# Optimization experiments

Measured on AMD Instinct MI355X. Metric: run time of the kernel, lower is better.

## Reference

```python
import jax, jax.numpy as jnp
import numpy as np

EPS = 1e-08


def _d_hat(d, mask, eps=EPS):
    # d: [B,N,H,W] float, mask: [B,N,H,W] bool
    B, N, H, W = mask.shape
    flat_d = d.reshape(B * N, H * W)
    flat_m = mask.reshape(B * N, H * W)
    cnt = flat_m.sum(axis=1)  # [BN] int
    # masked median: push invalid entries to +inf, sort, pick lower-median index
    sorted_v = jnp.sort(jnp.where(flat_m, flat_d, jnp.inf), axis=1)
    idx = jnp.maximum((cnt - 1) // 2, 0)
    med = jnp.take_along_axis(sorted_v, idx[:, None], axis=1)[:, 0]
    med = jnp.where(cnt > 0, med, jnp.zeros_like(med))  # empty mask -> median 0
    cnt_f = jnp.maximum(cnt, 1).astype(d.dtype)
    # masked MAD scale (mean abs deviation over valid pixels) + eps
    abs_sum = (jnp.abs(flat_d - med[:, None]) * flat_m).sum(axis=1)
    sc = jnp.where(cnt > 0, abs_sum / cnt_f + eps, jnp.full_like(abs_sum, eps))
    d_hat = (flat_d - med[:, None]) / sc[:, None]
    return d_hat.reshape(B, N, H, W)


def _avg_pool(x, k):
    # matches F.avg_pool2d(x, k, stride=k): crop to full windows, mean per kxk block
    B, N, H, W = x.shape
    Hk, Wk = H // k, W // k
    xc = x[..., : Hk * k, : Wk * k].reshape(B, N, Hk, k, Wk, k)
    return xc.mean(axis=(3, 5))


def _grad_loss(pred, target, mask):
    total = jnp.asarray(0.0, pred.dtype)
    mf = mask.astype(pred.dtype)
    for s in range(4):
        if s == 0:
            p, t, m = pred, target, mask
        else:
            k = 2 ** s
            p = _avg_pool(pred, k)
            t = _avg_pool(target, k)
            m = _avg_pool(mf, k) > 0  # .bool() of pooled float mask
        diff = p - t
        gx = jnp.abs(diff[..., :, 1:] - diff[..., :, :-1])
        gy = jnp.abs(diff[..., 1:, :] - diff[..., :-1, :])
        mx = m[..., :, 1:] & m[..., :, :-1]
        my = m[..., 1:, :] & m[..., :-1, :]
        lx = (gx * mx).sum() / jnp.maximum(mx.sum(), 1).astype(pred.dtype)
        ly = (gy * my).sum() / jnp.maximum(my.sum(), 1).astype(pred.dtype)
        total = total + lx + ly
    return total / 4


def setup_inputs() -> dict:
    key = jax.random.key(0)
    k1, k2, k3 = jax.random.split(key, 3)
    B, N, H, W = 4, 16, 518, 518
    pred = jax.random.normal(k1, (B, N, H, W), dtype=jnp.float32)
    y = jax.random.normal(k2, (B, N, H, W), dtype=jnp.float32)
    masks_squeezed = jax.random.bernoulli(k3, 0.9, (B, N, H, W))
    return {"pred": pred, "y": y, "masks_squeezed": masks_squeezed}


def reference(pred, y, masks_squeezed):
    mask = masks_squeezed.astype(bool)
    pred_hat = _d_hat(pred, mask)
    y_hat = _d_hat(y, mask)
    rho = jnp.abs(pred_hat - y_hat) * mask  # rho[~mask] = 0
    valid = jnp.maximum(mask.sum(axis=(2, 3)).astype(pred.dtype), 1.0)
    loss_ssi = (rho.sum(axis=(2, 3)) / valid).mean()
    loss_grad = _grad_loss(pred_hat, y_hat, mask)
    return loss_ssi + 0.5 * loss_grad
```

## Files before the change

kernel.cpp:

```cpp
#include <hip/hip_runtime.h>
#include <stdint.h>

typedef unsigned int u32;
typedef unsigned long long u64;
typedef unsigned char u8;

#define NIMG 64
#define W0   518
#define H0   518
#define HW   268324
#define HW4  67081
#define BPI  32
#define NB0  33
#define N1 67081
#define N2 16641
#define N3 4096
#define CAP 32768
#define LCAP 1536

#define OFF_HFB   0ULL
#define OFF_CNT   1048576ULL
#define OFF_CCNT  1048832ULL
#define OFF_CCNT2 1049344ULL
#define OFF_NBL   1049856ULL
#define OFF_OK    1050368ULL
#define OFF_SELP  1050880ULL
#define OFF_SELR  1051392ULL
#define OFF_NLT   1051904ULL
#define OFF_STOT  1052416ULL
#define OFF_SBL   1053440ULL
#define OFF_SLTFB 1054464ULL
#define OFF_RHO   1055488ULL
#define OFF_GI0   1056000ULL
#define OFF_GI1   1058048ULL
#define OFF_GI2   1060096ULL
#define OFF_GI3   1062144ULL
#define SMALL_END 1064192ULL
#define OFF_MED   1064192ULL
#define OFF_SCI   1064704ULL
#define OFF_SELW  1065216ULL
#define OFF_CAND  1067008ULL
#define OFF_MU8   (OFF_CAND + 16777216ULL)
#define OFF_P1    (OFF_MU8 + 17172736ULL)
#define OFF_M1    (OFF_P1 + 17172736ULL)
#define OFF_P2    (OFF_M1 + 4293184ULL)
#define OFF_M2    (OFF_P2 + 4260096ULL)
#define OFF_P3    (OFF_M2 + 1065024ULL)
#define OFF_M3    (OFF_P3 + 1048576ULL)

__device__ __forceinline__ u32 f2key(float f) {
  u32 u = __float_as_uint(f);
  return (u & 0x80000000u) ? ~u : (u | 0x80000000u);
}
__device__ __forceinline__ float key2f(u32 k) {
  u32 u = (k & 0x80000000u) ? (k & 0x7fffffffu) : ~k;
  return __uint_as_float(u);
}

__device__ void blk_rankfind(u32* h, int per, u32 target, bool enable,
                             u32* outBin, u32* outRank)
{
  int b0 = threadIdx.x * per;
  u32 s = 0;
  for (int j = 0; j < per; j++) s += h[b0 + j];
  u32 x = s;
  int lane = threadIdx.x & 63;
  for (int o = 1; o < 64; o <<= 1) {
    u32 v = __shfl_up(x, o, 64);
    if (lane >= o) x += v;
  }
  __shared__ u32 wsum[4];
  int wv = threadIdx.x >> 6;
  if (lane == 63) wsum[wv] = x;
  __syncthreads();
  u32 woff = 0;
  for (int w = 0; w < wv; w++) woff += wsum[w];
  u32 cum = woff + x - s;
  for (int j = 0; j < per; j++) {
    u32 v = h[b0 + j];
    if (enable && target >= cum && target < cum + v) { *outBin = (u32)(b0 + j); *outRank = target - cum; }
    cum += v;
  }
  __syncthreads();
}

__global__ __launch_bounds__(256) void k_sample(const float* __restrict__ p,
    const float* __restrict__ y, u32* __restrict__ selw)
{
  int t = blockIdx.x, img = t >> 1;
  const float* src = ((t & 1) ? y : p) + (size_t)img * HW;
  __shared__ u32 h[2048];
  __shared__ u32 bLo, rLo, bHi, rHi;
  if (threadIdx.x == 0) { bLo = 0; rLo = 0; bHi = 2047; rHi = 0; }
  for (int i = threadIdx.x; i < 2048; i += 256) h[i] = 0;
  __syncthreads();
  for (int j = 0; j < 16; j++) {
    int s = threadIdx.x * 16 + j;
    float v = src[s * 65 + 32];
    atomicAdd(&h[f2key(v) >> 21], 1u);
  }
  __syncthreads();
  blk_rankfind(h, 8, 1919u, true, &bLo, &rLo);
  blk_rankfind(h, 8, 2175u, true, &bHi, &rHi);
  if (threadIdx.x == 0) {
    u32 k0 = bLo << 21;
    u32 k1 = (bHi >= 2047u) ? 0xFFFFFFFFu : ((bHi + 1u) << 21);
    selw[2 * t + 0] = k0;
    selw[2 * t + 1] = k1;
  }
}

__global__ __launch_bounds__(256) void k_scan0(const float4* __restrict__ p,
    const float4* __restrict__ y, const int4* __restrict__ m,
    uchar4* __restrict__ mu4, const u32* __restrict__ selw,
    float* __restrict__ cand, u32* __restrict__ ccnt, u32* __restrict__ cnt,
    double* __restrict__ Stot, u32* __restrict__ Nbl, double* __restrict__ Sbl)
{
  __shared__ float capP[LCAP], capY[LCAP];
  __shared__ u32 nP, nY, baseP, baseY;
  if (threadIdx.x == 0) { nP = 0; nY = 0; }
  __syncthreads();
  int img = blockIdx.x / BPI, blk = blockIdx.x % BPI;
  u32 k0P = selw[img * 4 + 0], k1P = selw[img * 4 + 1];
  u32 k0Y = selw[img * 4 + 2], k1Y = selw[img * 4 + 3];
  const float4* pb = p + (size_t)img * HW4;
  const float4* yb = y + (size_t)img * HW4;
  const int4* mb = m + (size_t)img * HW4;
  uchar4* mo = mu4 + (size_t)img * HW4;
  int lc = 0, nB_p = 0, nB_y = 0;
  float sT_p = 0.f, sB_p = 0.f, sT_y = 0.f, sB_y = 0.f;
  for (int i = blk * 256 + threadIdx.x; i < HW4; i += BPI * 256) {
    float4 pv = pb[i], yv = yb[i];
    int4 mv = mb[i];
    uchar4 mw;
    mw.x = mv.x ? 1 : 0; mw.y = mv.y ? 1 : 0; mw.z = mv.z ? 1 : 0; mw.w = mv.w ? 1 : 0;
    mo[i] = mw;
#define SC(mm, vp, vy) if (mm) { lc++; \
      float v = vp; u32 k = f2key(v); sT_p += v; \
      if (k < k0P) { nB_p++; sB_p += v; } \
      else if (k < k1P) { u32 ix = atomicAdd(&nP, 1u); if (ix < LCAP) capP[ix] = v; } \
      v = vy; k = f2key(v); sT_y += v; \
      if (k < k0Y) { nB_y++; sB_y += v; } \
      else if (k < k1Y) { u32 ix = atomicAdd(&nY, 1u); if (ix < LCAP) capY[ix] = v; } }
    SC(mw.x, pv.x, yv.x) SC(mw.y, pv.y, yv.y) SC(mw.z, pv.z, yv.z) SC(mw.w, pv.w, yv.w)
#undef SC
  }
  __syncthreads();
  if (threadIdx.x == 0) {
    u32 np = nP, ny = nY;
    u32 addP = (np > (u32)LCAP) ? (u32)(CAP + 1) : np;
    u32 addY = (ny > (u32)LCAP) ? (u32)(CAP + 1) : ny;
    baseP = atomicAdd(&ccnt[img * 2 + 0], addP);
    baseY = atomicAdd(&ccnt[img * 2 + 1], addY);
  }
  __syncthreads();
  {
    u32 np = min(nP, (u32)LCAP), ny = min(nY, (u32)LCAP);
    float* cp = cand + (size_t)(img * 2 + 0) * CAP;
    float* cy = cand + (size_t)(img * 2 + 1) * CAP;
    for (u32 i = threadIdx.x; i < np; i += 256) { u32 g = baseP + i; if (g < CAP) cp[g] = capP[i]; }
    for (u32 i = threadIdx.x; i < ny; i += 256) { u32 g = baseY + i; if (g < CAP) cy[g] = capY[i]; }
  }
  double v0 = (double)sT_p, v1 = (double)sB_p, v2 = (double)sT_y, v3 = (double)sB_y;
  double v4 = (double)lc, v5 = (double)nB_p, v6 = (double)nB_y;
  for (int o = 32; o; o >>= 1) {
    v0 += __shfl_down(v0, o, 64); v1 += __shfl_down(v1, o, 64);
    v2 += __shfl_down(v2, o, 64); v3 += __shfl_down(v3, o, 64);
    v4 += __shfl_down(v4, o, 64); v5 += __shfl_down(v5, o, 64);
    v6 += __shfl_down(v6, o, 64);
  }
  __shared__ double sh[7][4];
  int lane = threadIdx.x & 63, wv = threadIdx.x >> 6;
  if (lane == 0) { sh[0][wv]=v0; sh[1][wv]=v1; sh[2][wv]=v2; sh[3][wv]=v3; sh[4][wv]=v4; sh[5][wv]=v5; sh[6][wv]=v6; }
  __syncthreads();
  if (threadIdx.x == 0) {
    double a[7];
    for (int k = 0; k < 7; k++) a[k] = sh[k][0] + sh[k][1] + sh[k][2] + sh[k][3];
    atomicAdd(&Stot[img * 2 + 0], a[0]);
    atomicAdd(&Sbl [img * 2 + 0], a[1]);
    atomicAdd(&Stot[img * 2 + 1], a[2]);
    atomicAdd(&Sbl [img * 2 + 1], a[3]);
    atomicAdd(&cnt[img], (u32)a[4]);
    atomicAdd(&Nbl[img * 2 + 0], (u32)a[5]);
    atomicAdd(&Nbl[img * 2 + 1], (u32)a[6]);
  }
}

__global__ __launch_bounds__(256) void k_med2(const float* __restrict__ cand,
    const u32* __restrict__ ccnt, const u32* __restrict__ cnt,
    const u32* __restrict__ Nbl, const double* __restrict__ Stot,
    const double* __restrict__ Sbl, const u32* __restrict__ selw,
    float* __restrict__ med, float* __restrict__ sci, u32* __restrict__ ok)
{
  int t = blockIdx.x, img = t >> 1;
  u32 c = cnt[img];
  if (c == 0) {
    if (threadIdx.x == 0) { med[t] = 0.f; sci[t] = 1e8f; ok[t] = 1; }
    return;
  }
  u32 ntot = ccnt[t];
  u32 target0 = (c - 1) >> 1;
  u32 nb = Nbl[t];
  bool valid = (ntot <= (u32)CAP) && (target0 >= nb) && ((target0 - nb) < ntot);
  if (!valid) { if (threadIdx.x == 0) ok[t] = 0; return; }
  u32 n = ntot;
  const float* cd = cand + (size_t)t * CAP;
  u32 k0 = selw[2 * t + 0], k1 = selw[2 * t + 1];
  __shared__ u32 h[2048];
  __shared__ u32 sBin, sRank;
  if (threadIdx.x == 0) { sBin = 0; sRank = 0; }
  u32 curLo = k0;
  u64 curR = (u64)k1 - (u64)k0;
  u32 tgt = target0 - nb;
  for (int pass = 0; pass < 3; pass++) {
    int s = 0;
    while (((curR - 1) >> s) >= 2048) s++;
    for (int i = threadIdx.x; i < 2048; i += 256) h[i] = 0;
    __syncthreads();
    for (u32 j = threadIdx.x; j < n; j += 256) {
      u32 k = f2key(cd[j]);
      if (k >= curLo && (u64)(k - curLo) < curR)
        atomicAdd(&h[(k - curLo) >> s], 1u);
    }
    __syncthreads();
    blk_rankfind(h, 8, tgt, true, &sBin, &sRank);
    curLo = curLo + (sBin << s);
    curR = (u64)1 << s;
    tgt = sRank;
    if (s == 0) break;
  }
  float m = key2f(curLo);
  u32 nlt2 = 0; float slt2 = 0.f;
  for (u32 j = threadIdx.x; j < n; j += 256) {
    float v = cd[j];
    if (v < m) { nlt2++; slt2 += v; }
  }
  double v0 = (double)nlt2, v1 = (double)slt2;
  for (int o = 32; o; o >>= 1) { v0 += __shfl_down(v0, o, 64); v1 += __shfl_down(v1, o, 64); }
  __shared__ double sh2[2][4];
  int lane = threadIdx.x & 63, wv = threadIdx.x >> 6;
  if (lane == 0) { sh2[0][wv] = v0; sh2[1][wv] = v1; }
  __syncthreads();
  if (threadIdx.x == 0) {
    double nl = (double)nb + sh2[0][0] + sh2[0][1] + sh2[0][2] + sh2[0][3];
    double sl = Sbl[t] + sh2[1][0] + sh2[1][1] + sh2[1][2] + sh2[1][3];
    double md = (double)m;
    double mad = Stot[t] + 2.0 * md * nl - 2.0 * sl - md * (double)c;
    double sc = mad / (double)c + 1e-8;
    med[t] = m; sci[t] = (float)(1.0 / sc); ok[t] = 1;
  }
}

__global__ __launch_bounds__(256) void k_fb_hist(const float4* __restrict__ p,
    const float4* __restrict__ y, const uchar4* __restrict__ mu,
    const u32* __restrict__ ok, u32* __restrict__ hist)
{
  int img = blockIdx.x / BPI, blk = blockIdx.x % BPI;
  if (ok[img * 2 + 0] && ok[img * 2 + 1]) return;
  __shared__ u32 h[4096];
  for (int i = threadIdx.x; i < 4096; i += 256) h[i] = 0;
  __syncthreads();
  const float4* pb = p + (size_t)img * HW4;
  const float4* yb = y + (size_t)img * HW4;
  const uchar4* mb = mu + (size_t)img * HW4;
  for (int i = blk * 256 + threadIdx.x; i < HW4; i += BPI * 256) {
    float4 pv = pb[i], yv = yb[i];
    uchar4 mv = mb[i];
#define FH(mm, vp, vy) if (mm) { atomicAdd(&h[f2key(vp) >> 21], 1u); atomicAdd(&h[2048u + (f2key(vy) >> 21)], 1u); }
    FH(mv.x, pv.x, yv.x) FH(mv.y, pv.y, yv.y) FH(mv.z, pv.z, yv.z) FH(mv.w, pv.w, yv.w)
#undef FH
  }
  __syncthreads();
  u32* gh = hist + (size_t)img * 4096;
  for (int b = threadIdx.x; b < 4096; b += 256) if (h[b]) atomicAdd(&gh[b], h[b]);
}

__global__ __launch_bounds__(256) void k_fb_sel(const u32* __restrict__ hist,
    const u32* __restrict__ cnt, const u32* __restrict__ ok,
    u32* __restrict__ selp, u32* __restrict__ selr, u32* __restrict__ nlt)
{
  int t = blockIdx.x, img = t >> 1;
  if (ok[t]) return;
  __shared__ u32 hh[2048];
  __shared__ u32 sBin, sRank;
  if (threadIdx.x == 0) { sBin = 0; sRank = 0; }
  const u32* gh = hist + (size_t)t * 2048;
  for (int i = threadIdx.x; i < 2048; i += 256) hh[i] = gh[i];
  __syncthreads();
  u32 c = cnt[img];
  u32 target = c ? ((c - 1) >> 1) : 0u;
  blk_rankfind(hh, 8, target, c != 0, &sBin, &sRank);
  if (threadIdx.x == 0) { selp[t] = sBin; selr[t] = sRank; nlt[t] = target - sRank; }
}

__global__ __launch_bounds__(256) void k_fb_compact(const float4* __restrict__ p,
    const float4* __restrict__ y, const uchar4* __restrict__ mu,
    const u32* __restrict__ ok, const u32* __restrict__ selp,
    float* __restrict__ cand, u32* __restrict__ ccnt2, double* __restrict__ Sltfb)
{
  int img = blockIdx.x / BPI, blk = blockIdx.x % BPI;
  if (ok[img * 2 + 0] && ok[img * 2 + 1]) return;
  u32 binP = selp[img * 2 + 0], binY = selp[img * 2 + 1];
  const float4* pb = p + (size_t)img * HW4;
  const float4* yb = y + (size_t)img * HW4;
  const uchar4* mb = mu + (size_t)img * HW4;
  float* cp = cand + (size_t)(img * 2 + 0) * CAP;
  float* cyv = cand + (size_t)(img * 2 + 1) * CAP;
  u32* ccP = &ccnt2[img * 2 + 0];
  u32* ccY = &ccnt2[img * 2 + 1];
  float sLp = 0.f, sLy = 0.f;
  for (int i = blk * 256 + threadIdx.x; i < HW4; i += BPI * 256) {
    float4 pv = pb[i], yv = yb[i];
    uchar4 mv = mb[i];
#define FC(mm, vp, vy) if (mm) { \
      float v = vp; u32 b = f2key(v) >> 21; \
      if (b < binP) sLp += v; else if (b == binP) { u32 ix = atomicAdd(ccP, 1u); if (ix < CAP) cp[ix] = v; } \
      v = vy; b = f2key(v) >> 21; \
      if (b < binY) sLy += v; else if (b == binY) { u32 ix = atomicAdd(ccY, 1u); if (ix < CAP) cyv[ix] = v; } }
    FC(mv.x, pv.x, yv.x) FC(mv.y, pv.y, yv.y) FC(mv.z, pv.z, yv.z) FC(mv.w, pv.w, yv.w)
#undef FC
  }
  double v0 = (double)sLp, v1 = (double)sLy;
  for (int o = 32; o; o >>= 1) { v0 += __shfl_down(v0, o, 64); v1 += __shfl_down(v1, o, 64); }
  __shared__ double sh[2][4];
  int lane = threadIdx.x & 63, wv = threadIdx.x >> 6;
  if (lane == 0) { sh[0][wv] = v0; sh[1][wv] = v1; }
  __syncthreads();
  if (threadIdx.x == 0) {
    atomicAdd(&Sltfb[img * 2 + 0], sh[0][0] + sh[0][1] + sh[0][2] + sh[0][3]);
    atomicAdd(&Sltfb[img * 2 + 1], sh[1][0] + sh[1][1] + sh[1][2] + sh[1][3]);
  }
}

__global__ __launch_bounds__(256) void k_fb_med(const float* __restrict__ cand,
    const u32* __restrict__ ccnt2, const u32* __restrict__ cnt,
    const u32* __restrict__ ok, const u32* __restrict__ selp,
    const u32* __restrict__ selr, const u32* __restrict__ nlt,
    const double* __restrict__ Stot, const double* __restrict__ Sltfb,
    float* __restrict__ med, float* __restrict__ sci)
{
  int t = blockIdx.x, img = t >> 1;
  if (ok[t]) return;
  u32 c = cnt[img];
  u32 n = ccnt2[t]; if (n > CAP) n = CAP;
  const float* cd = cand + (size_t)t * CAP;
  u32 target = selr[t];
  __shared__ u32 h[2048];
  __shared__ u32 sBin, sRank;
  if (threadIdx.x == 0) { sBin = 0; sRank = 0; }
  u32 curLo = selp[t] << 21;
  u64 curR = (u64)1 << 21;
  u32 tgt = target;
  for (int pass = 0; pass < 2; pass++) {
    int s = 0;
    while (((curR - 1) >> s) >= 2048) s++;
    for (int i = threadIdx.x; i < 2048; i += 256) h[i] = 0;
    __syncthreads();
    for (u32 j = threadIdx.x; j < n; j += 256) {
      u32 k = f2key(cd[j]);
      if (k >= curLo && (u64)(k - curLo) < curR)
        atomicAdd(&h[(k - curLo) >> s], 1u);
    }
    __syncthreads();
    blk_rankfind(h, 8, tgt, c != 0, &sBin, &sRank);
    curLo = curLo + (sBin << s);
    curR = (u64)1 << s;
    tgt = sRank;
    if (s == 0) break;
  }
  float m = key2f(curLo);
  u32 nlt2 = 0; float slt2 = 0.f;
  for (u32 j = threadIdx.x; j < n; j += 256) {
    float v = cd[j];
    if (v < m) { nlt2++; slt2 += v; }
  }
  double v0 = (double)nlt2, v1 = (double)slt2;
  for (int o = 32; o; o >>= 1) { v0 += __shfl_down(v0, o, 64); v1 += __shfl_down(v1, o, 64); }
  __shared__ double sh2[2][4];
  int lane = threadIdx.x & 63, wv = threadIdx.x >> 6;
  if (lane == 0) { sh2[0][wv] = v0; sh2[1][wv] = v1; }
  __syncthreads();
  if (threadIdx.x == 0) {
    if (c) {
      double nl = (double)nlt[t] + sh2[0][0] + sh2[0][1] + sh2[0][2] + sh2[0][3];
      double sl = Sltfb[t] + sh2[1][0] + sh2[1][1] + sh2[1][2] + sh2[1][3];
      double md = (double)m;
      double mad = Stot[t] + 2.0 * md * nl - 2.0 * sl - md * (double)c;
      double sc = mad / (double)c + 1e-8;
      med[t] = m; sci[t] = (float)(1.0 / sc);
    } else { med[t] = 0.f; sci[t] = 1e8f; }
  }
}

__global__ __launch_bounds__(320) void k_fuse0(const float* __restrict__ p,
    const float* __restrict__ y, const u8* __restrict__ mu,
    const float* __restrict__ medv, const float* __restrict__ sciv,
    float* __restrict__ P1, u8* __restrict__ M1,
    double* __restrict__ rho, double* __restrict__ gI)
{
  int img = blockIdx.x / NB0, band = blockIdx.x % NB0;
  float mp = medv[img * 2 + 0], my = medv[img * 2 + 1];
  float ap = sciv[img * 2 + 0], ay = sciv[img * 2 + 1];
  const float* pb = p + (size_t)img * HW;
  const float* yb = y + (size_t)img * HW;
  const u8*   mb = mu + (size_t)img * HW;
  int ra = band * 16;
  int rb = min(ra + 16, H0);
  int rend = (rb < H0) ? rb + 1 : H0;
  int oc = threadIdx.x;
  bool act = oc < 259;
  int cc = act ? 2 * oc : 516;
  bool vn = act && (2 * oc + 2 < W0);
  int lane = threadIdx.x & 63;
  bool edge = (lane == 63);
  float gx = 0.f, gy = 0.f, rr = 0.f;
  int cx = 0, cy = 0;
  float pd0 = 0.f, pd1 = 0.f; u8 pm0 = 0, pm1 = 0;
  size_t rbase = (size_t)ra * W0;
  float2 pv = *(const float2*)(pb + rbase + cc);
  float2 yv = *(const float2*)(yb + rbase + cc);
  uchar2 mv = *(const uchar2*)(mb + rbase + cc);
  for (int r = ra; r < rend; ++r) {
    float2 pn2 = pv, yn2 = yv; uchar2 mn2 = mv;
    if (r + 1 < rend) {
      size_t nb2 = (size_t)(r + 1) * W0;
      pn2 = *(const float2*)(pb + nb2 + cc);
      yn2 = *(const float2*)(yb + nb2 + cc);
      mn2 = *(const uchar2*)(mb + nb2 + cc);
    }
    bool core = r < rb;
    float d0 = (pv.x - mp) * ap - (yv.x - my) * ay;
    float d1 = (pv.y - mp) * ap - (yv.y - my) * ay;
    u8 m0 = mv.x, m1 = mv.y;
    float dn = __shfl_down(d0, 1, 64);
    int mn = __shfl_down((int)m0, 1, 64);
    if (vn && edge) {
      size_t a = (size_t)r * W0 + (size_t)cc + 2;
      float pnb = pb[a], ynb = yb[a];
      dn = (pnb - mp) * ap - (ynb - my) * ay;
      mn = mb[a];
    }
    if (act) {
      float f0 = (float)m0, f1 = (float)m1;
      if (core) {
        gx += f0 * f1 * fabsf(d1 - d0); cx += (int)(m0 & m1);
        if (vn) { float fn = (float)mn; gx += f1 * fn * fabsf(dn - d1); cx += (m1 && mn) ? 1 : 0; }
        rr += f0 * fabsf(d0) + f1 * fabsf(d1);
      }
      if (r > ra) {
        gy += f0 * (float)pm0 * fabsf(d0 - pd0); cy += (int)(m0 & pm0);
        gy += f1 * (float)pm1 * fabsf(d1 - pd1); cy += (int)(m1 & pm1);
      }
      if (core && (r & 1)) {
        size_t o = (size_t)img * N1 + (size_t)(r >> 1) * 259 + oc;
        P1[o] = 0.25f * (pd0 + pd1 + d0 + d1);
        M1[o] = (u8)((pm0 | pm1 | m0 | m1) ? 1 : 0);
      }
    }
    pd0 = d0; pd1 = d1; pm0 = m0; pm1 = m1;
    pv = pn2; yv = yn2; mv = mn2;
  }
  double v0 = (double)gx, v1 = (double)cx, v2 = (double)gy, v3 = (double)cy, v4 = (double)rr;
  for (int o = 32; o; o >>= 1) {
    v0 += __shfl_down(v0, o, 64); v1 += __shfl_down(v1, o, 64);
    v2 += __shfl_down(v2, o, 64); v3 += __shfl_down(v3, o, 64);
    v4 += __shfl_down(v4, o, 64);
  }
  __shared__ double sh[5][5];
  int wv = threadIdx.x >> 6;
  if (lane == 0) { sh[0][wv] = v0; sh[1][wv] = v1; sh[2][wv] = v2; sh[3][wv] = v3; sh[4][wv] = v4; }
  __syncthreads();
  if (threadIdx.x == 0) {
    double a0 = 0, a1 = 0, a2 = 0, a3 = 0, a4 = 0;
    for (int w = 0; w < 5; w++) { a0 += sh[0][w]; a1 += sh[1][w]; a2 += sh[2][w]; a3 += sh[3][w]; a4 += sh[4][w]; }
    atomicAdd(&gI[img * 4 + 0], a0);
    atomicAdd(&gI[img * 4 + 1], a1);
    atomicAdd(&gI[img * 4 + 2], a2);
    atomicAdd(&gI[img * 4 + 3], a3);
    atomicAdd(&rho[img], a4);
  }
}

__global__ void k_gp(const float* __restrict__ Pin,
    const u8* __restrict__ Min, float* __restrict__ Pout, u8* __restrict__ Mout,
    int Win, int Hin, int Wout, int Hout, int nb, double* __restrict__ gI)
{
  int img = blockIdx.x / nb, band = blockIdx.x % nb;
  int npixI = Win * Hin, npixO = Wout * Hout;
  const float* pb = Pin + (size_t)img * npixI;
  const u8* mb = Min + (size_t)img * npixI;
  int poolEnd = 2 * Hout;
  int ra = band * 16;
  int rb = min(ra + 16, poolEnd);
  int rbx = (band == nb - 1) ? Hin : rb;
  int rend = (rbx < Hin) ? rbx + 1 : Hin;
  float gx = 0.f, gy = 0.f;
  int cx = 0, cy = 0;
  int oc = threadIdx.x;
  if (oc < Wout) {
    int c0 = 2 * oc, c1 = c0 + 1, cn = c0 + 2;
    bool vn = cn < Win;
    bool gyn = vn && (cn >= 2 * Wout);
    float pd0 = 0.f, pd1 = 0.f, pdn = 0.f;
    u8 pm0 = 0, pm1 = 0, pmn = 0;
    for (int r = ra; r < rend; ++r) {
      bool core = r < rbx;
      int base = r * Win;
      float d0 = pb[base + c0], d1 = pb[base + c1];
      u8 m0 = mb[base + c0], m1 = mb[base + c1];
      float dn = 0.f; u8 mn = 0;
      if (vn) { dn = pb[base + cn]; mn = mb[base + cn]; }
      if (core) {
        if (m0 & m1) { gx += fabsf(d1 - d0); cx++; }
        if (vn && (m1 & mn)) { gx += fabsf(dn - d1); cx++; }
      }
      if (r > ra) {
        if (m0 & pm0) { gy += fabsf(d0 - pd0); cy++; }
        if (m1 & pm1) { gy += fabsf(d1 - pd1); cy++; }
        if (gyn && (mn & pmn)) { gy += fabsf(dn - pdn); cy++; }
      }
      if (core && (r & 1) && r < poolEnd) {
        size_t o = (size_t)img * npixO + (size_t)(r >> 1) * Wout + oc;
        Pout[o] = 0.25f * (pd0 + pd1 + d0 + d1);
        Mout[o] = (u8)((pm0 | pm1 | m0 | m1) ? 1 : 0);
      }
      pd0 = d0; pd1 = d1; pdn = dn; pm0 = m0; pm1 = m1; pmn = mn;
    }
  }
  double v0 = (double)gx, v1 = (double)cx, v2 = (double)gy, v3 = (double)cy;
  for (int o = 32; o; o >>= 1) {
    v0 += __shfl_down(v0, o, 64); v1 += __shfl_down(v1, o, 64);
    v2 += __shfl_down(v2, o, 64); v3 += __shfl_down(v3, o, 64);
  }
  __shared__ double sh[4][4];
  int lane = threadIdx.x & 63, wv = threadIdx.x >> 6;
  int nw = (blockDim.x + 63) >> 6;
  if (lane == 0) { sh[0][wv] = v0; sh[1][wv] = v1; sh[2][wv] = v2; sh[3][wv] = v3; }
  __syncthreads();
  if (threadIdx.x == 0) {
    double a0 = 0, a1 = 0, a2 = 0, a3 = 0;
    for (int w = 0; w < nw; w++) { a0 += sh[0][w]; a1 += sh[1][w]; a2 += sh[2][w]; a3 += sh[3][w]; }
    atomicAdd(&gI[img * 4 + 0], a0);
    atomicAdd(&gI[img * 4 + 1], a1);
    atomicAdd(&gI[img * 4 + 2], a2);
    atomicAdd(&gI[img * 4 + 3], a3);
  }
}

__global__ __launch_bounds__(256) void k_grad3(const float* __restrict__ P,
    const u8* __restrict__ M, double* __restrict__ gI)
{
  int t = blockIdx.x * 256 + threadIdx.x;
  int img = t >> 12, px = t & 4095;
  int col = px & 63;
  const float* Pi = P + ((size_t)img << 12);
  const u8* Mi = M + ((size_t)img << 12);
  float gx = 0.f, gy = 0.f;
  int cx = 0, cy = 0;
  float dc = Pi[px];
  u8 mc = Mi[px];
  if (col < 63 && mc && Mi[px + 1]) { gx = fabsf(Pi[px + 1] - dc); cx = 1; }
  if (px < 4032 && mc && Mi[px + 64]) { gy = fabsf(Pi[px + 64] - dc); cy = 1; }
  double v0 = (double)gx, v1 = (double)cx, v2 = (double)gy, v3 = (double)cy;
  for (int o = 32; o; o >>= 1) {
    v0 += __shfl_down(v0, o, 64); v1 += __shfl_down(v1, o, 64);
    v2 += __shfl_down(v2, o, 64); v3 += __shfl_down(v3, o, 64);
  }
  __shared__ double sh[4][4];
  int lane = threadIdx.x & 63, wv = threadIdx.x >> 6;
  if (lane == 0) { sh[0][wv] = v0; sh[1][wv] = v1; sh[2][wv] = v2; sh[3][wv] = v3; }
  __syncthreads();
  if (threadIdx.x == 0) {
    atomicAdd(&gI[img * 4 + 0], sh[0][0] + sh[0][1] + sh[0][2] + sh[0][3]);
    atomicAdd(&gI[img * 4 + 1], sh[1][0] + sh[1][1] + sh[1][2] + sh[1][3]);
    atomicAdd(&gI[img * 4 + 2], sh[2][0] + sh[2][1] + sh[2][2] + sh[2][3]);
    atomicAdd(&gI[img * 4 + 3], sh[3][0] + sh[3][1] + sh[3][2] + sh[3][3]);
  }
}

__global__ void k_final(const double* __restrict__ rho, const u32* __restrict__ cnt,
    const double* __restrict__ gI0, const double* __restrict__ gI1,
    const double* __restrict__ gI2, const double* __restrict__ gI3,
    float* __restrict__ out)
{
  int i = threadIdx.x;
  double v[17];
  double c = cnt[i] ? (double)cnt[i] : 1.0;
  v[0] = rho[i] / c;
  for (int j = 0; j < 4; j++) {
    v[1 + 0 * 4 + j] = gI0[i * 4 + j];
    v[1 + 1 * 4 + j] = gI1[i * 4 + j];
    v[1 + 2 * 4 + j] = gI2[i * 4 + j];
    v[1 + 3 * 4 + j] = gI3[i * 4 + j];
  }
  for (int o = 32; o; o >>= 1)
    for (int k = 0; k < 17; k++) v[k] += __shfl_down(v[k], o, 64);
  if (i == 0) {
    double ssi = v[0] / (double)NIMG;
    double g = 0.0;
    for (int s = 0; s < 4; s++) {
      double gxs = v[1 + s * 4 + 0], cxs = v[1 + s * 4 + 1];
      double gys = v[1 + s * 4 + 2], cys = v[1 + s * 4 + 3];
      g += gxs / (cxs > 1.0 ? cxs : 1.0);
      g += gys / (cys > 1.0 ? cys : 1.0);
    }
    g /= 4.0;
    out[0] = (float)(ssi + 0.5 * g);
  }
}

extern "C" void kernel_launch(void* const* d_in, const int* in_sizes, int n_in,
                              void* d_out, int out_size, void* d_ws, size_t ws_size,
                              hipStream_t stream) {
  (void)in_sizes; (void)n_in; (void)out_size; (void)ws_size;
  const float4* p4 = (const float4*)d_in[0];
  const float4* y4 = (const float4*)d_in[1];
  const int4* m4 = (const int4*)d_in[2];
  const float* pf = (const float*)d_in[0];
  const float* yf = (const float*)d_in[1];
  u8* ws = (u8*)d_ws;

  u32*    Hfb  = (u32*)(ws + OFF_HFB);
  u32*    cnt  = (u32*)(ws + OFF_CNT);
  u32*    ccnt = (u32*)(ws + OFF_CCNT);
  u32*    ccnt2= (u32*)(ws + OFF_CCNT2);
  u32*    Nbl  = (u32*)(ws + OFF_NBL);
  u32*    ok   = (u32*)(ws + OFF_OK);
  u32*    selp = (u32*)(ws + OFF_SELP);
  u32*    selr = (u32*)(ws + OFF_SELR);
  u32*    nlt  = (u32*)(ws + OFF_NLT);
  double* Stot = (double*)(ws + OFF_STOT);
  double* Sbl  = (double*)(ws + OFF_SBL);
  double* Sltfb= (double*)(ws + OFF_SLTFB);
  double* rho  = (double*)(ws + OFF_RHO);
  double* gI0  = (double*)(ws + OFF_GI0);
  double* gI1  = (double*)(ws + OFF_GI1);
  double* gI2  = (double*)(ws + OFF_GI2);
  double* gI3  = (double*)(ws + OFF_GI3);
  float*  med  = (float*)(ws + OFF_MED);
  float*  sci  = (float*)(ws + OFF_SCI);
  u32*    selw = (u32*)(ws + OFF_SELW);
  float*  cand = (float*)(ws + OFF_CAND);
  u8*     mu8  = (u8*)(ws + OFF_MU8);
  float*  P1   = (float*)(ws + OFF_P1);
  u8*     M1   = (u8*)(ws + OFF_M1);
  float*  P2   = (float*)(ws + OFF_P2);
  u8*     M2   = (u8*)(ws + OFF_M2);
  float*  P3   = (float*)(ws + OFF_P3);
  u8*     M3   = (u8*)(ws + OFF_M3);

  hipMemsetAsync(d_ws, 0, SMALL_END, stream);

  k_sample<<<128, 256, 0, stream>>>(pf, yf, selw);
  k_scan0<<<NIMG * BPI, 256, 0, stream>>>(p4, y4, m4, (uchar4*)mu8, selw, cand, ccnt, cnt, Stot, Nbl, Sbl);
  k_med2<<<128, 256, 0, stream>>>(cand, ccnt, cnt, Nbl, Stot, Sbl, selw, med, sci, ok);

  k_fb_hist<<<NIMG * BPI, 256, 0, stream>>>(p4, y4, (const uchar4*)mu8, ok, Hfb);
  k_fb_sel<<<128, 256, 0, stream>>>(Hfb, cnt, ok, selp, selr, nlt);
  k_fb_compact<<<NIMG * BPI, 256, 0, stream>>>(p4, y4, (const uchar4*)mu8, ok, selp, cand, ccnt2, Sltfb);
  k_fb_med<<<128, 256, 0, stream>>>(cand, ccnt2, cnt, ok, selp, selr, nlt, Stot, Sltfb, med, sci);

  k_fuse0<<<NIMG * NB0, 320, 0, stream>>>(pf, yf, mu8, med, sci, P1, M1, rho, gI0);
  k_gp<<<NIMG * 17, 192, 0, stream>>>(P1, M1, P2, M2, 259, 259, 129, 129, 17, gI1);
  k_gp<<<NIMG * 8, 64, 0, stream>>>(P2, M2, P3, M3, 129, 129, 64, 64, 8, gI2);
  k_grad3<<<1024, 256, 0, stream>>>(P3, M3, gI3);

  k_final<<<1, 64, 0, stream>>>(rho, cnt, gI0, gI1, gI2, gI3, (float*)d_out);
}
```

Measured before the change: 380.2 us.

## Fold fallback median into k_med2, fuse last pool levels, drop memset

Removes the separate fallback kernels (histogram, select, compact, median) and moves the fallback path inside k_med2. Fuses the last pooling level with the level-3 gradient into one kernel, which drops the P3/M3 buffers and the k_grad3 launch. Replaces the workspace memset with zeroing inside k_sample, compares float thresholds directly in k_scan0 with a 2x unrolled load loop, and deepens the row prefetch in k_fuse0. This cuts launches and passes over memory, at the risk that a single-block fallback in k_med2 is slow when it is triggered.

```diff
diff --git a/kernel.cpp b/kernel.cpp
--- a/kernel.cpp
+++ b/kernel.cpp
@@ -14,39 +14,30 @@
 #define NB0  33
 #define N1 67081
 #define N2 16641
-#define N3 4096
 #define CAP 32768
-#define LCAP 1536
-
-#define OFF_HFB   0ULL
-#define OFF_CNT   1048576ULL
-#define OFF_CCNT  1048832ULL
-#define OFF_CCNT2 1049344ULL
-#define OFF_NBL   1049856ULL
-#define OFF_OK    1050368ULL
-#define OFF_SELP  1050880ULL
-#define OFF_SELR  1051392ULL
-#define OFF_NLT   1051904ULL
-#define OFF_STOT  1052416ULL
-#define OFF_SBL   1053440ULL
-#define OFF_SLTFB 1054464ULL
-#define OFF_RHO   1055488ULL
-#define OFF_GI0   1056000ULL
-#define OFF_GI1   1058048ULL
-#define OFF_GI2   1060096ULL
-#define OFF_GI3   1062144ULL
-#define SMALL_END 1064192ULL
-#define OFF_MED   1064192ULL
-#define OFF_SCI   1064704ULL
-#define OFF_SELW  1065216ULL
-#define OFF_CAND  1067008ULL
+#define LCAP 1024
+
+#define OFF_CNT   0ULL
+#define OFF_CCNT  256ULL
+#define OFF_NBL   768ULL
+#define OFF_RHO   1280ULL
+#define OFF_STOT  1792ULL
+#define OFF_SBL   2816ULL
+#define OFF_GI0   3840ULL
+#define OFF_GI1   5888ULL
+#define OFF_GI2   7936ULL
+#define OFF_GI3   9984ULL
+#define ZERO_END  12032ULL
+#define OFF_MED   12032ULL
+#define OFF_SCI   12544ULL
+#define OFF_SELW  13056ULL
+#define OFF_SWF   14080ULL
+#define OFF_CAND  15360ULL
 #define OFF_MU8   (OFF_CAND + 16777216ULL)
 #define OFF_P1    (OFF_MU8 + 17172736ULL)
 #define OFF_M1    (OFF_P1 + 17172736ULL)
 #define OFF_P2    (OFF_M1 + 4293184ULL)
 #define OFF_M2    (OFF_P2 + 4260096ULL)
-#define OFF_P3    (OFF_M2 + 1065024ULL)
-#define OFF_M3    (OFF_P3 + 1048576ULL)
 
 __device__ __forceinline__ u32 f2key(float f) {
   u32 u = __float_as_uint(f);
@@ -57,12 +48,11 @@
   return __uint_as_float(u);
 }
 
-__device__ void blk_rankfind(u32* h, int per, u32 target, bool enable,
-                             u32* outBin, u32* outRank)
-{
-  int b0 = threadIdx.x * per;
+__device__ void blk_rankfind(u32* h, u32 target, bool enable, u32* outBin, u32* outRank)
+{
+  int b0 = threadIdx.x * 8;
   u32 s = 0;
-  for (int j = 0; j < per; j++) s += h[b0 + j];
+  for (int j = 0; j < 8; j++) s += h[b0 + j];
   u32 x = s;
   int lane = threadIdx.x & 63;
   for (int o = 1; o < 64; o <<= 1) {
@@ -76,7 +66,7 @@
   u32 woff = 0;
   for (int w = 0; w < wv; w++) woff += wsum[w];
   u32 cum = woff + x - s;
-  for (int j = 0; j < per; j++) {
+  for (int j = 0; j < 8; j++) {
     u32 v = h[b0 + j];
     if (enable && target >= cum && target < cum + v) { *outBin = (u32)(b0 + j); *outRank = target - cum; }
     cum += v;
@@ -85,13 +75,17 @@
 }
 
 __global__ __launch_bounds__(256) void k_sample(const float* __restrict__ p,
-    const float* __restrict__ y, u32* __restrict__ selw)
+    const float* __restrict__ y, u32* __restrict__ selw, float* __restrict__ swf,
+    u32* __restrict__ zbase)
 {
   int t = blockIdx.x, img = t >> 1;
+  if (t == 0) {
+    for (int i = threadIdx.x; i < 3008; i += 256) zbase[i] = 0;
+  }
   const float* src = ((t & 1) ? y : p) + (size_t)img * HW;
   __shared__ u32 h[2048];
-  __shared__ u32 bLo, rLo, bHi, rHi;
-  if (threadIdx.x == 0) { bLo = 0; rLo = 0; bHi = 2047; rHi = 0; }
+  __shared__ u32 bLo, rT, bHi;
+  if (threadIdx.x == 0) { bLo = 0; bHi = 2047; }
   for (int i = threadIdx.x; i < 2048; i += 256) h[i] = 0;
   __syncthreads();
   for (int j = 0; j < 16; j++) {
@@ -100,19 +94,23 @@
     atomicAdd(&h[f2key(v) >> 21], 1u);
   }
   __syncthreads();
-  blk_rankfind(h, 8, 1919u, true, &bLo, &rLo);
-  blk_rankfind(h, 8, 2175u, true, &bHi, &rHi);
+  blk_rankfind(h, 1919u, true, &bLo, &rT);
+  blk_rankfind(h, 2175u, true, &bHi, &rT);
   if (threadIdx.x == 0) {
     u32 k0 = bLo << 21;
     u32 k1 = (bHi >= 2047u) ? 0xFFFFFFFFu : ((bHi + 1u) << 21);
     selw[2 * t + 0] = k0;
     selw[2 * t + 1] = k1;
+    float f0 = (k0 <= 0x007FFFFFu) ? __uint_as_float(0xFF800000u) : key2f(k0);
+    float f1 = (k1 >= 0xFF800000u) ? __uint_as_float(0x7F800000u) : key2f(k1);
+    swf[2 * t + 0] = f0;
+    swf[2 * t + 1] = f1;
   }
 }
 
 __global__ __launch_bounds__(256) void k_scan0(const float4* __restrict__ p,
     const float4* __restrict__ y, const int4* __restrict__ m,
-    uchar4* __restrict__ mu4, const u32* __restrict__ selw,
+    uchar4* __restrict__ mu4, const float* __restrict__ swf,
     float* __restrict__ cand, u32* __restrict__ ccnt, u32* __restrict__ cnt,
     double* __restrict__ Stot, u32* __restrict__ Nbl, double* __restrict__ Sbl)
 {
@@ -121,30 +119,45 @@
   if (threadIdx.x == 0) { nP = 0; nY = 0; }
   __syncthreads();
   int img = blockIdx.x / BPI, blk = blockIdx.x % BPI;
-  u32 k0P = selw[img * 4 + 0], k1P = selw[img * 4 + 1];
-  u32 k0Y = selw[img * 4 + 2], k1Y = selw[img * 4 + 3];
+  float f0P = swf[img * 4 + 0], f1P = swf[img * 4 + 1];
+  float f0Y = swf[img * 4 + 2], f1Y = swf[img * 4 + 3];
   const float4* pb = p + (size_t)img * HW4;
   const float4* yb = y + (size_t)img * HW4;
   const int4* mb = m + (size_t)img * HW4;
   uchar4* mo = mu4 + (size_t)img * HW4;
-  int lc = 0, nB_p = 0, nB_y = 0;
-  float sT_p = 0.f, sB_p = 0.f, sT_y = 0.f, sB_y = 0.f;
-  for (int i = blk * 256 + threadIdx.x; i < HW4; i += BPI * 256) {
-    float4 pv = pb[i], yv = yb[i];
-    int4 mv = mb[i];
-    uchar4 mw;
-    mw.x = mv.x ? 1 : 0; mw.y = mv.y ? 1 : 0; mw.z = mv.z ? 1 : 0; mw.w = mv.w ? 1 : 0;
-    mo[i] = mw;
-#define SC(mm, vp, vy) if (mm) { lc++; \
-      float v = vp; u32 k = f2key(v); sT_p += v; \
-      if (k < k0P) { nB_p++; sB_p += v; } \
-      else if (k < k1P) { u32 ix = atomicAdd(&nP, 1u); if (ix < LCAP) capP[ix] = v; } \
-      v = vy; k = f2key(v); sT_y += v; \
-      if (k < k0Y) { nB_y++; sB_y += v; } \
-      else if (k < k1Y) { u32 ix = atomicAdd(&nY, 1u); if (ix < LCAP) capY[ix] = v; } }
-    SC(mw.x, pv.x, yv.x) SC(mw.y, pv.y, yv.y) SC(mw.z, pv.z, yv.z) SC(mw.w, pv.w, yv.w)
-#undef SC
-  }
+  int lc = 0, nBp = 0, nBy = 0;
+  float sTp = 0.f, sBp = 0.f, sTy = 0.f, sBy = 0.f;
+
+#define PEL(mm, vp, vy) if (mm) { lc++; \
+      sTp += vp; \
+      if (vp < f0P) { nBp++; sBp += vp; } \
+      else if (vp < f1P) { u32 ix = atomicAdd(&nP, 1u); if (ix < LCAP) capP[ix] = vp; } \
+      sTy += vy; \
+      if (vy < f0Y) { nBy++; sBy += vy; } \
+      else if (vy < f1Y) { u32 ix = atomicAdd(&nY, 1u); if (ix < LCAP) capY[ix] = vy; } }
+#define PGRP(idx) { \
+      float4 pv = pb[idx]; float4 yv = yb[idx]; int4 mv = mb[idx]; \
+      uchar4 mw; mw.x = mv.x ? 1 : 0; mw.y = mv.y ? 1 : 0; mw.z = mv.z ? 1 : 0; mw.w = mv.w ? 1 : 0; \
+      mo[idx] = mw; \
+      PEL(mw.x, pv.x, yv.x) PEL(mw.y, pv.y, yv.y) PEL(mw.z, pv.z, yv.z) PEL(mw.w, pv.w, yv.w) }
+
+  const int S = BPI * 256;
+  int i = blk * 256 + threadIdx.x;
+  for (; i + S < HW4; i += 2 * S) {
+    float4 pa = pb[i], pc = pb[i + S];
+    float4 ya = yb[i], yc = yb[i + S];
+    int4 ma = mb[i], mc = mb[i + S];
+    uchar4 wa, wc;
+    wa.x = ma.x ? 1 : 0; wa.y = ma.y ? 1 : 0; wa.z = ma.z ? 1 : 0; wa.w = ma.w ? 1 : 0;
+    wc.x = mc.x ? 1 : 0; wc.y = mc.y ? 1 : 0; wc.z = mc.z ? 1 : 0; wc.w = mc.w ? 1 : 0;
+    mo[i] = wa; mo[i + S] = wc;
+    PEL(wa.x, pa.x, ya.x) PEL(wa.y, pa.y, ya.y) PEL(wa.z, pa.z, ya.z) PEL(wa.w, pa.w, ya.w)
+    PEL(wc.x, pc.x, yc.x) PEL(wc.y, pc.y, yc.y) PEL(wc.z, pc.z, yc.z) PEL(wc.w, pc.w, yc.w)
+  }
+  if (i < HW4) PGRP(i)
+#undef PGRP
+#undef PEL
+
   __syncthreads();
   if (threadIdx.x == 0) {
     u32 np = nP, ny = nY;
@@ -158,11 +171,11 @@
     u32 np = min(nP, (u32)LCAP), ny = min(nY, (u32)LCAP);
     float* cp = cand + (size_t)(img * 2 + 0) * CAP;
     float* cy = cand + (size_t)(img * 2 + 1) * CAP;
-    for (u32 i = threadIdx.x; i < np; i += 256) { u32 g = baseP + i; if (g < CAP) cp[g] = capP[i]; }
-    for (u32 i = threadIdx.x; i < ny; i += 256) { u32 g = baseY + i; if (g < CAP) cy[g] = capY[i]; }
-  }
-  double v0 = (double)sT_p, v1 = (double)sB_p, v2 = (double)sT_y, v3 = (double)sB_y;
-  double v4 = (double)lc, v5 = (double)nB_p, v6 = (double)nB_y;
+    for (u32 k = threadIdx.x; k < np; k += 256) { u32 g = baseP + k; if (g < CAP) cp[g] = capP[k]; }
+    for (u32 k = threadIdx.x; k < ny; k += 256) { u32 g = baseY + k; if (g < CAP) cy[g] = capY[k]; }
+  }
+  double v0 = (double)sTp, v1 = (double)sBp, v2 = (double)sTy, v3 = (double)sBy;
+  double v4 = (double)lc, v5 = (double)nBp, v6 = (double)nBy;
   for (int o = 32; o; o >>= 1) {
     v0 += __shfl_down(v0, o, 64); v1 += __shfl_down(v1, o, 64);
     v2 += __shfl_down(v2, o, 64); v3 += __shfl_down(v3, o, 64);
@@ -190,205 +203,108 @@
     const u32* __restrict__ ccnt, const u32* __restrict__ cnt,
     const u32* __restrict__ Nbl, const double* __restrict__ Stot,
     const double* __restrict__ Sbl, const u32* __restrict__ selw,
-    float* __restrict__ med, float* __restrict__ sci, u32* __restrict__ ok)
+    const float* __restrict__ pf, const float* __restrict__ yf,
+    const u8* __restrict__ mu8, float* __restrict__ med, float* __restrict__ sci)
 {
   int t = blockIdx.x, img = t >> 1;
   u32 c = cnt[img];
   if (c == 0) {
-    if (threadIdx.x == 0) { med[t] = 0.f; sci[t] = 1e8f; ok[t] = 1; }
+    if (threadIdx.x == 0) { med[t] = 0.f; sci[t] = 1e8f; }
     return;
   }
   u32 ntot = ccnt[t];
   u32 target0 = (c - 1) >> 1;
   u32 nb = Nbl[t];
   bool valid = (ntot <= (u32)CAP) && (target0 >= nb) && ((target0 - nb) < ntot);
-  if (!valid) { if (threadIdx.x == 0) ok[t] = 0; return; }
-  u32 n = ntot;
-  const float* cd = cand + (size_t)t * CAP;
-  u32 k0 = selw[2 * t + 0], k1 = selw[2 * t + 1];
   __shared__ u32 h[2048];
   __shared__ u32 sBin, sRank;
   if (threadIdx.x == 0) { sBin = 0; sRank = 0; }
-  u32 curLo = k0;
-  u64 curR = (u64)k1 - (u64)k0;
-  u32 tgt = target0 - nb;
-  for (int pass = 0; pass < 3; pass++) {
-    int s = 0;
-    while (((curR - 1) >> s) >= 2048) s++;
-    for (int i = threadIdx.x; i < 2048; i += 256) h[i] = 0;
+  int lane = threadIdx.x & 63, wv = threadIdx.x >> 6;
+  __shared__ double sh2[2][4];
+
+  if (valid) {
+    u32 n = ntot;
+    const float* cd = cand + (size_t)t * CAP;
+    u32 curLo = selw[2 * t + 0];
+    u64 curR = (u64)selw[2 * t + 1] - (u64)curLo;
+    u32 tgt = target0 - nb;
+    for (int pass = 0; pass < 3; pass++) {
+      int s = 0;
+      while (((curR - 1) >> s) >= 2048) s++;
+      for (int i = threadIdx.x; i < 2048; i += 256) h[i] = 0;
+      __syncthreads();
+      for (u32 j = threadIdx.x; j < n; j += 256) {
+        u32 k = f2key(cd[j]);
+        if (k >= curLo && (u64)(k - curLo) < curR)
+          atomicAdd(&h[(k - curLo) >> s], 1u);
+      }
+      __syncthreads();
+      blk_rankfind(h, tgt, true, &sBin, &sRank);
+      curLo = curLo + (sBin << s);
+      curR = (u64)1 << s;
+      tgt = sRank;
+      if (s == 0) break;
+    }
+    float mv = key2f(curLo);
+    u32 nlt2 = 0; float slt2 = 0.f;
+    for (u32 j = threadIdx.x; j < n; j += 256) {
+      float v = cd[j];
+      if (v < mv) { nlt2++; slt2 += v; }
+    }
+    double v0 = (double)nlt2, v1 = (double)slt2;
+    for (int o = 32; o; o >>= 1) { v0 += __shfl_down(v0, o, 64); v1 += __shfl_down(v1, o, 64); }
+    if (lane == 0) { sh2[0][wv] = v0; sh2[1][wv] = v1; }
     __syncthreads();
-    for (u32 j = threadIdx.x; j < n; j += 256) {
-      u32 k = f2key(cd[j]);
-      if (k >= curLo && (u64)(k - curLo) < curR)
-        atomicAdd(&h[(k - curLo) >> s], 1u);
-    }
-    __syncthreads();
-    blk_rankfind(h, 8, tgt, true, &sBin, &sRank);
-    curLo = curLo + (sBin << s);
-    curR = (u64)1 << s;
-    tgt = sRank;
-    if (s == 0) break;
-  }
-  float m = key2f(curLo);
-  u32 nlt2 = 0; float slt2 = 0.f;
-  for (u32 j = threadIdx.x; j < n; j += 256) {
-    float v = cd[j];
-    if (v < m) { nlt2++; slt2 += v; }
-  }
-  double v0 = (double)nlt2, v1 = (double)slt2;
-  for (int o = 32; o; o >>= 1) { v0 += __shfl_down(v0, o, 64); v1 += __shfl_down(v1, o, 64); }
-  __shared__ double sh2[2][4];
-  int lane = threadIdx.x & 63, wv = threadIdx.x >> 6;
-  if (lane == 0) { sh2[0][wv] = v0; sh2[1][wv] = v1; }
-  __syncthreads();
-  if (threadIdx.x == 0) {
-    double nl = (double)nb + sh2[0][0] + sh2[0][1] + sh2[0][2] + sh2[0][3];
-    double sl = Sbl[t] + sh2[1][0] + sh2[1][1] + sh2[1][2] + sh2[1][3];
-    double md = (double)m;
-    double mad = Stot[t] + 2.0 * md * nl - 2.0 * sl - md * (double)c;
-    double sc = mad / (double)c + 1e-8;
-    med[t] = m; sci[t] = (float)(1.0 / sc); ok[t] = 1;
-  }
-}
-
-__global__ __launch_bounds__(256) void k_fb_hist(const float4* __restrict__ p,
-    const float4* __restrict__ y, const uchar4* __restrict__ mu,
-    const u32* __restrict__ ok, u32* __restrict__ hist)
-{
-  int img = blockIdx.x / BPI, blk = blockIdx.x % BPI;
-  if (ok[img * 2 + 0] && ok[img * 2 + 1]) return;
-  __shared__ u32 h[4096];
-  for (int i = threadIdx.x; i < 4096; i += 256) h[i] = 0;
-  __syncthreads();
-  const float4* pb = p + (size_t)img * HW4;
-  const float4* yb = y + (size_t)img * HW4;
-  const uchar4* mb = mu + (size_t)img * HW4;
-  for (int i = blk * 256 + threadIdx.x; i < HW4; i += BPI * 256) {
-    float4 pv = pb[i], yv = yb[i];
-    uchar4 mv = mb[i];
-#define FH(mm, vp, vy) if (mm) { atomicAdd(&h[f2key(vp) >> 21], 1u); atomicAdd(&h[2048u + (f2key(vy) >> 21)], 1u); }
-    FH(mv.x, pv.x, yv.x) FH(mv.y, pv.y, yv.y) FH(mv.z, pv.z, yv.z) FH(mv.w, pv.w, yv.w)
-#undef FH
-  }
-  __syncthreads();
-  u32* gh = hist + (size_t)img * 4096;
-  for (int b = threadIdx.x; b < 4096; b += 256) if (h[b]) atomicAdd(&gh[b], h[b]);
-}
-
-__global__ __launch_bounds__(256) void k_fb_sel(const u32* __restrict__ hist,
-    const u32* __restrict__ cnt, const u32* __restrict__ ok,
-    u32* __restrict__ selp, u32* __restrict__ selr, u32* __restrict__ nlt)
-{
-  int t = blockIdx.x, img = t >> 1;
-  if (ok[t]) return;
-  __shared__ u32 hh[2048];
-  __shared__ u32 sBin, sRank;
-  if (threadIdx.x == 0) { sBin = 0; sRank = 0; }
-  const u32* gh = hist + (size_t)t * 2048;
-  for (int i = threadIdx.x; i < 2048; i += 256) hh[i] = gh[i];
-  __syncthreads();
-  u32 c = cnt[img];
-  u32 target = c ? ((c - 1) >> 1) : 0u;
-  blk_rankfind(hh, 8, target, c != 0, &sBin, &sRank);
-  if (threadIdx.x == 0) { selp[t] = sBin; selr[t] = sRank; nlt[t] = target - sRank; }
-}
-
-__global__ __launch_bounds__(256) void k_fb_compact(const float4* __restrict__ p,
-    const float4* __restrict__ y, const uchar4* __restrict__ mu,
-    const u32* __restrict__ ok, const u32* __restrict__ selp,
-    float* __restrict__ cand, u32* __restrict__ ccnt2, double* __restrict__ Sltfb)
-{
-  int img = blockIdx.x / BPI, blk = blockIdx.x % BPI;
-  if (ok[img * 2 + 0] && ok[img * 2 + 1]) return;
-  u32 binP = selp[img * 2 + 0], binY = selp[img * 2 + 1];
-  const float4* pb = p + (size_t)img * HW4;
-  const float4* yb = y + (size_t)img * HW4;
-  const uchar4* mb = mu + (size_t)img * HW4;
-  float* cp = cand + (size_t)(img * 2 + 0) * CAP;
-  float* cyv = cand + (size_t)(img * 2 + 1) * CAP;
-  u32* ccP = &ccnt2[img * 2 + 0];
-  u32* ccY = &ccnt2[img * 2 + 1];
-  float sLp = 0.f, sLy = 0.f;
-  for (int i = blk * 256 + threadIdx.x; i < HW4; i += BPI * 256) {
-    float4 pv = pb[i], yv = yb[i];
-    uchar4 mv = mb[i];
-#define FC(mm, vp, vy) if (mm) { \
-      float v = vp; u32 b = f2key(v) >> 21; \
-      if (b < binP) sLp += v; else if (b == binP) { u32 ix = atomicAdd(ccP, 1u); if (ix < CAP) cp[ix] = v; } \
-      v = vy; b = f2key(v) >> 21; \
-      if (b < binY) sLy += v; else if (b == binY) { u32 ix = atomicAdd(ccY, 1u); if (ix < CAP) cyv[ix] = v; } }
-    FC(mv.x, pv.x, yv.x) FC(mv.y, pv.y, yv.y) FC(mv.z, pv.z, yv.z) FC(mv.w, pv.w, yv.w)
-#undef FC
-  }
-  double v0 = (double)sLp, v1 = (double)sLy;
-  for (int o = 32; o; o >>= 1) { v0 += __shfl_down(v0, o, 64); v1 += __shfl_down(v1, o, 64); }
-  __shared__ double sh[2][4];
-  int lane = threadIdx.x & 63, wv = threadIdx.x >> 6;
-  if (lane == 0) { sh[0][wv] = v0; sh[1][wv] = v1; }
-  __syncthreads();
-  if (threadIdx.x == 0) {
-    atomicAdd(&Sltfb[img * 2 + 0], sh[0][0] + sh[0][1] + sh[0][2] + sh[0][3]);
-    atomicAdd(&Sltfb[img * 2 + 1], sh[1][0] + sh[1][1] + sh[1][2] + sh[1][3]);
-  }
-}
-
-__global__ __launch_bounds__(256) void k_fb_med(const float* __restrict__ cand,
-    const u32* __restrict__ ccnt2, const u32* __restrict__ cnt,
-    const u32* __restrict__ ok, const u32* __restrict__ selp,
-    const u32* __restrict__ selr, const u32* __restrict__ nlt,
-    const double* __restrict__ Stot, const double* __restrict__ Sltfb,
-    float* __restrict__ med, float* __restrict__ sci)
-{
-  int t = blockIdx.x, img = t >> 1;
-  if (ok[t]) return;
-  u32 c = cnt[img];
-  u32 n = ccnt2[t]; if (n > CAP) n = CAP;
-  const float* cd = cand + (size_t)t * CAP;
-  u32 target = selr[t];
-  __shared__ u32 h[2048];
-  __shared__ u32 sBin, sRank;
-  if (threadIdx.x == 0) { sBin = 0; sRank = 0; }
-  u32 curLo = selp[t] << 21;
-  u64 curR = (u64)1 << 21;
-  u32 tgt = target;
-  for (int pass = 0; pass < 2; pass++) {
-    int s = 0;
-    while (((curR - 1) >> s) >= 2048) s++;
-    for (int i = threadIdx.x; i < 2048; i += 256) h[i] = 0;
-    __syncthreads();
-    for (u32 j = threadIdx.x; j < n; j += 256) {
-      u32 k = f2key(cd[j]);
-      if (k >= curLo && (u64)(k - curLo) < curR)
-        atomicAdd(&h[(k - curLo) >> s], 1u);
-    }
-    __syncthreads();
-    blk_rankfind(h, 8, tgt, c != 0, &sBin, &sRank);
-    curLo = curLo + (sBin << s);
-    curR = (u64)1 << s;
-    tgt = sRank;
-    if (s == 0) break;
-  }
-  float m = key2f(curLo);
-  u32 nlt2 = 0; float slt2 = 0.f;
-  for (u32 j = threadIdx.x; j < n; j += 256) {
-    float v = cd[j];
-    if (v < m) { nlt2++; slt2 += v; }
-  }
-  double v0 = (double)nlt2, v1 = (double)slt2;
-  for (int o = 32; o; o >>= 1) { v0 += __shfl_down(v0, o, 64); v1 += __shfl_down(v1, o, 64); }
-  __shared__ double sh2[2][4];
-  int lane = threadIdx.x & 63, wv = threadIdx.x >> 6;
-  if (lane == 0) { sh2[0][wv] = v0; sh2[1][wv] = v1; }
-  __syncthreads();
-  if (threadIdx.x == 0) {
-    if (c) {
-      double nl = (double)nlt[t] + sh2[0][0] + sh2[0][1] + sh2[0][2] + sh2[0][3];
-      double sl = Sltfb[t] + sh2[1][0] + sh2[1][1] + sh2[1][2] + sh2[1][3];
-      double md = (double)m;
+    if (threadIdx.x == 0) {
+      double nl = (double)nb + sh2[0][0] + sh2[0][1] + sh2[0][2] + sh2[0][3];
+      double sl = Sbl[t] + sh2[1][0] + sh2[1][1] + sh2[1][2] + sh2[1][3];
+      double md = (double)mv;
       double mad = Stot[t] + 2.0 * md * nl - 2.0 * sl - md * (double)c;
       double sc = mad / (double)c + 1e-8;
-      med[t] = m; sci[t] = (float)(1.0 / sc);
-    } else { med[t] = 0.f; sci[t] = 1e8f; }
+      med[t] = mv; sci[t] = (float)(1.0 / sc);
+    }
+  } else {
+    const float* src = ((t & 1) ? yf : pf) + (size_t)img * HW;
+    const u8* mk = mu8 + (size_t)img * HW;
+    u32 curLo = 0; u64 curR = (u64)1 << 32; u32 tgt = target0;
+    for (int pass = 0; pass < 4; pass++) {
+      int s = 0;
+      while (((curR - 1) >> s) >= 2048) s++;
+      for (int i = threadIdx.x; i < 2048; i += 256) h[i] = 0;
+      __syncthreads();
+      for (u32 j = threadIdx.x; j < (u32)HW; j += 256) {
+        if (mk[j]) {
+          u32 k = f2key(src[j]);
+          if (k >= curLo && (u64)(k - curLo) < curR)
+            atomicAdd(&h[(k - curLo) >> s], 1u);
+        }
+      }
+      __syncthreads();
+      blk_rankfind(h, tgt, true, &sBin, &sRank);
+      curLo = curLo + (sBin << s);
+      curR = (u64)1 << s;
+      tgt = sRank;
+      if (s == 0) break;
+    }
+    float mv = key2f(curLo);
+    double nl = 0.0, sl = 0.0;
+    for (u32 j = threadIdx.x; j < (u32)HW; j += 256) {
+      if (mk[j]) {
+        float v = src[j];
+        if (v < mv) { nl += 1.0; sl += (double)v; }
+      }
+    }
+    for (int o = 32; o; o >>= 1) { nl += __shfl_down(nl, o, 64); sl += __shfl_down(sl, o, 64); }
+    if (lane == 0) { sh2[0][wv] = nl; sh2[1][wv] = sl; }
+    __syncthreads();
+    if (threadIdx.x == 0) {
+      double nlT = sh2[0][0] + sh2[0][1] + sh2[0][2] + sh2[0][3];
+      double slT = sh2[1][0] + sh2[1][1] + sh2[1][2] + sh2[1][3];
+      double md = (double)mv;
+      double mad = Stot[t] + 2.0 * md * nlT - 2.0 * slT - md * (double)c;
+      double sc = mad / (double)c + 1e-8;
+      med[t] = mv; sci[t] = (float)(1.0 / sc);
+    }
   }
 }
 
@@ -416,22 +332,26 @@
   float gx = 0.f, gy = 0.f, rr = 0.f;
   int cx = 0, cy = 0;
   float pd0 = 0.f, pd1 = 0.f; u8 pm0 = 0, pm1 = 0;
-  size_t rbase = (size_t)ra * W0;
-  float2 pv = *(const float2*)(pb + rbase + cc);
-  float2 yv = *(const float2*)(yb + rbase + cc);
-  uchar2 mv = *(const uchar2*)(mb + rbase + cc);
+  float2 pv0, yv0, pv1, yv1;
+  uchar2 mv0, mv1;
+  {
+    size_t a0 = (size_t)ra * W0 + cc;
+    pv0 = *(const float2*)(pb + a0); yv0 = *(const float2*)(yb + a0); mv0 = *(const uchar2*)(mb + a0);
+    if (ra + 1 < rend) {
+      size_t a1 = a0 + W0;
+      pv1 = *(const float2*)(pb + a1); yv1 = *(const float2*)(yb + a1); mv1 = *(const uchar2*)(mb + a1);
+    } else { pv1 = pv0; yv1 = yv0; mv1 = mv0; }
+  }
   for (int r = ra; r < rend; ++r) {
-    float2 pn2 = pv, yn2 = yv; uchar2 mn2 = mv;
-    if (r + 1 < rend) {
-      size_t nb2 = (size_t)(r + 1) * W0;
-      pn2 = *(const float2*)(pb + nb2 + cc);
-      yn2 = *(const float2*)(yb + nb2 + cc);
-      mn2 = *(const uchar2*)(mb + nb2 + cc);
+    float2 pv2 = pv1, yv2 = yv1; uchar2 mv2 = mv1;
+    if (r + 2 < rend) {
+      size_t a2 = (size_t)(r + 2) * W0 + cc;
+      pv2 = *(const float2*)(pb + a2); yv2 = *(const float2*)(yb + a2); mv2 = *(const uchar2*)(mb + a2);
     }
     bool core = r < rb;
-    float d0 = (pv.x - mp) * ap - (yv.x - my) * ay;
-    float d1 = (pv.y - mp) * ap - (yv.y - my) * ay;
-    u8 m0 = mv.x, m1 = mv.y;
+    float d0 = (pv0.x - mp) * ap - (yv0.x - my) * ay;
+    float d1 = (pv0.y - mp) * ap - (yv0.y - my) * ay;
+    u8 m0 = mv0.x, m1 = mv0.y;
     float dn = __shfl_down(d0, 1, 64);
     int mn = __shfl_down((int)m0, 1, 64);
     if (vn && edge) {
@@ -458,7 +378,8 @@
       }
     }
     pd0 = d0; pd1 = d1; pm0 = m0; pm1 = m1;
-    pv = pn2; yv = yn2; mv = mn2;
+    pv0 = pv1; yv0 = yv1; mv0 = mv1;
+    pv1 = pv2; yv1 = yv2; mv1 = mv2;
   }
   double v0 = (double)gx, v1 = (double)cx, v2 = (double)gy, v3 = (double)cy, v4 = (double)rr;
   for (int o = 32; o; o >>= 1) {
@@ -547,34 +468,69 @@
   }
 }
 
-__global__ __launch_bounds__(256) void k_grad3(const float* __restrict__ P,
-    const u8* __restrict__ M, double* __restrict__ gI)
-{
-  int t = blockIdx.x * 256 + threadIdx.x;
-  int img = t >> 12, px = t & 4095;
-  int col = px & 63;
-  const float* Pi = P + ((size_t)img << 12);
-  const u8* Mi = M + ((size_t)img << 12);
-  float gx = 0.f, gy = 0.f;
-  int cx = 0, cy = 0;
-  float dc = Pi[px];
-  u8 mc = Mi[px];
-  if (col < 63 && mc && Mi[px + 1]) { gx = fabsf(Pi[px + 1] - dc); cx = 1; }
-  if (px < 4032 && mc && Mi[px + 64]) { gy = fabsf(Pi[px + 64] - dc); cy = 1; }
-  double v0 = (double)gx, v1 = (double)cx, v2 = (double)gy, v3 = (double)cy;
-  for (int o = 32; o; o >>= 1) {
-    v0 += __shfl_down(v0, o, 64); v1 += __shfl_down(v1, o, 64);
-    v2 += __shfl_down(v2, o, 64); v3 += __shfl_down(v3, o, 64);
-  }
-  __shared__ double sh[4][4];
-  int lane = threadIdx.x & 63, wv = threadIdx.x >> 6;
-  if (lane == 0) { sh[0][wv] = v0; sh[1][wv] = v1; sh[2][wv] = v2; sh[3][wv] = v3; }
-  __syncthreads();
+__global__ __launch_bounds__(64) void k_gp_last(const float* __restrict__ Pin,
+    const u8* __restrict__ Min, double* __restrict__ gI2v, double* __restrict__ gI3v)
+{
+  const int Win = 129, Hin = 129, Wout = 64, nb = 8;
+  int img = blockIdx.x / nb, band = blockIdx.x % nb;
+  const float* pb = Pin + (size_t)img * (Win * Hin);
+  const u8* mb = Min + (size_t)img * (Win * Hin);
+  int ra = band * 16;
+  int rb = min(ra + 16, 128);
+  int rbx = (band == nb - 1) ? Hin : rb;
+  int rend2 = (band < nb - 1) ? (ra + 18) : Hin;
+  float gx = 0.f, gy = 0.f; int cx = 0, cy = 0;
+  float ogx = 0.f, ogy = 0.f; int ocx = 0, ocy = 0;
+  int oc = threadIdx.x;
+  int c0 = 2 * oc, c1 = c0 + 1, cn = c0 + 2;
+  bool vn = cn < Win;
+  bool gyn = vn && (cn >= 2 * Wout);
+  float pd0 = 0.f, pd1 = 0.f, pdn = 0.f;
+  u8 pm0 = 0, pm1 = 0, pmn = 0;
+  float ppo = 0.f; int pmo = 0; bool havePrev = false;
+  for (int r = ra; r < rend2; ++r) {
+    int base = r * Win;
+    float d0 = pb[base + c0], d1 = pb[base + c1];
+    u8 m0 = mb[base + c0], m1 = mb[base + c1];
+    float dn = 0.f; u8 mn = 0;
+    if (vn) { dn = pb[base + cn]; mn = mb[base + cn]; }
+    if (r < rbx) {
+      if (m0 & m1) { gx += fabsf(d1 - d0); cx++; }
+      if (vn && (m1 & mn)) { gx += fabsf(dn - d1); cx++; }
+    }
+    if (r > ra && r <= rb) {
+      if (m0 & pm0) { gy += fabsf(d0 - pd0); cy++; }
+      if (m1 & pm1) { gy += fabsf(d1 - pd1); cy++; }
+      if (gyn && (mn & pmn)) { gy += fabsf(dn - pdn); cy++; }
+    }
+    if (r & 1) {
+      bool owned = r < rb;
+      bool halo = (r == rb + 1);
+      if (owned || halo) {
+        float po = 0.25f * (pd0 + pd1 + d0 + d1);
+        int mo = (pm0 | pm1 | m0 | m1) ? 1 : 0;
+        float pon = __shfl_down(po, 1, 64);
+        int mon = __shfl_down(mo, 1, 64);
+        if (owned && oc < 63 && mo && mon) { ogx += fabsf(pon - po); ocx++; }
+        if (havePrev && mo && pmo) { ogy += fabsf(po - ppo); ocy++; }
+        ppo = po; pmo = mo; havePrev = true;
+      }
+    }
+    pd0 = d0; pd1 = d1; pdn = dn; pm0 = m0; pm1 = m1; pmn = mn;
+  }
+  double v[8] = {(double)gx, (double)cx, (double)gy, (double)cy,
+                 (double)ogx, (double)ocx, (double)ogy, (double)ocy};
+  for (int o = 32; o; o >>= 1)
+    for (int k = 0; k < 8; k++) v[k] += __shfl_down(v[k], o, 64);
   if (threadIdx.x == 0) {
-    atomicAdd(&gI[img * 4 + 0], sh[0][0] + sh[0][1] + sh[0][2] + sh[0][3]);
-    atomicAdd(&gI[img * 4 + 1], sh[1][0] + sh[1][1] + sh[1][2] + sh[1][3]);
-    atomicAdd(&gI[img * 4 + 2], sh[2][0] + sh[2][1] + sh[2][2] + sh[2][3]);
-    atomicAdd(&gI[img * 4 + 3], sh[3][0] + sh[3][1] + sh[3][2] + sh[3][3]);
+    atomicAdd(&gI2v[img * 4 + 0], v[0]);
+    atomicAdd(&gI2v[img * 4 + 1], v[1]);
+    atomicAdd(&gI2v[img * 4 + 2], v[2]);
+    atomicAdd(&gI2v[img * 4 + 3], v[3]);
+    atomicAdd(&gI3v[img * 4 + 0], v[4]);
+    atomicAdd(&gI3v[img * 4 + 1], v[5]);
+    atomicAdd(&gI3v[img * 4 + 2], v[6]);
+    atomicAdd(&gI3v[img * 4 + 3], v[7]);
   }
 }
 
@@ -620,19 +576,12 @@
   const float* yf = (const float*)d_in[1];
   u8* ws = (u8*)d_ws;
 
-  u32*    Hfb  = (u32*)(ws + OFF_HFB);
   u32*    cnt  = (u32*)(ws + OFF_CNT);
   u32*    ccnt = (u32*)(ws + OFF_CCNT);
-  u32*    ccnt2= (u32*)(ws + OFF_CCNT2);
   u32*    Nbl  = (u32*)(ws + OFF_NBL);
-  u32*    ok   = (u32*)(ws + OFF_OK);
-  u32*    selp = (u32*)(ws + OFF_SELP);
-  u32*    selr = (u32*)(ws + OFF_SELR);
-  u32*    nlt  = (u32*)(ws + OFF_NLT);
+  double* rho  = (double*)(ws + OFF_RHO);
   double* Stot = (double*)(ws + OFF_STOT);
   double* Sbl  = (double*)(ws + OFF_SBL);
-  double* Sltfb= (double*)(ws + OFF_SLTFB);
-  double* rho  = (double*)(ws + OFF_RHO);
   double* gI0  = (double*)(ws + OFF_GI0);
   double* gI1  = (double*)(ws + OFF_GI1);
   double* gI2  = (double*)(ws + OFF_GI2);
@@ -640,30 +589,19 @@
   float*  med  = (float*)(ws + OFF_MED);
   float*  sci  = (float*)(ws + OFF_SCI);
   u32*    selw = (u32*)(ws + OFF_SELW);
+  float*  swf  = (float*)(ws + OFF_SWF);
   float*  cand = (float*)(ws + OFF_CAND);
   u8*     mu8  = (u8*)(ws + OFF_MU8);
   float*  P1   = (float*)(ws + OFF_P1);
   u8*     M1   = (u8*)(ws + OFF_M1);
   float*  P2   = (float*)(ws + OFF_P2);
   u8*     M2   = (u8*)(ws + OFF_M2);
-  float*  P3   = (float*)(ws + OFF_P3);
-  u8*     M3   = (u8*)(ws + OFF_M3);
-
-  hipMemsetAsync(d_ws, 0, SMALL_END, stream);
-
-  k_sample<<<128, 256, 0, stream>>>(pf, yf, selw);
-  k_scan0<<<NIMG * BPI, 256, 0, stream>>>(p4, y4, m4, (uchar4*)mu8, selw, cand, ccnt, cnt, Stot, Nbl, Sbl);
-  k_med2<<<128, 256, 0, stream>>>(cand, ccnt, cnt, Nbl, Stot, Sbl, selw, med, sci, ok);
-
-  k_fb_hist<<<NIMG * BPI, 256, 0, stream>>>(p4, y4, (const uchar4*)mu8, ok, Hfb);
-  k_fb_sel<<<128, 256, 0, stream>>>(Hfb, cnt, ok, selp, selr, nlt);
-  k_fb_compact<<<NIMG * BPI, 256, 0, stream>>>(p4, y4, (const uchar4*)mu8, ok, selp, cand, ccnt2, Sltfb);
-  k_fb_med<<<128, 256, 0, stream>>>(cand, ccnt2, cnt, ok, selp, selr, nlt, Stot, Sltfb, med, sci);
-
+
+  k_sample<<<128, 256, 0, stream>>>(pf, yf, selw, swf, (u32*)ws);
+  k_scan0<<<NIMG * BPI, 256, 0, stream>>>(p4, y4, m4, (uchar4*)mu8, swf, cand, ccnt, cnt, Stot, Nbl, Sbl);
+  k_med2<<<128, 256, 0, stream>>>(cand, ccnt, cnt, Nbl, Stot, Sbl, selw, pf, yf, mu8, med, sci);
   k_fuse0<<<NIMG * NB0, 320, 0, stream>>>(pf, yf, mu8, med, sci, P1, M1, rho, gI0);
   k_gp<<<NIMG * 17, 192, 0, stream>>>(P1, M1, P2, M2, 259, 259, 129, 129, 17, gI1);
-  k_gp<<<NIMG * 8, 64, 0, stream>>>(P2, M2, P3, M3, 129, 129, 64, 64, 8, gI2);
-  k_grad3<<<1024, 256, 0, stream>>>(P3, M3, gI3);
-
+  k_gp_last<<<NIMG * 8, 64, 0, stream>>>(P2, M2, gI2, gI3);
   k_final<<<1, 64, 0, stream>>>(rho, cnt, gI0, gI1, gI2, gI3, (float*)d_out);
 }
```

Result: faster. 366.1 us (-3.7%).
